# Performance work log

Hardware: AMD Instinct MI355X
Metric: run time of the kernel (lower is better)

## Reference

```python
import jax, jax.numpy as jnp
import numpy as np

N, E = 50000, 800000
IN, HID, EMB, PROJ = 256, 256, 128, 128


def setup_inputs() -> dict:
    key = jax.random.key(0)
    ks = jax.random.split(key, 10)
    s_in = 1.0 / np.sqrt(IN)
    s_hid = 1.0 / np.sqrt(HID)
    s_emb = 1.0 / np.sqrt(EMB)
    s_proj = 1.0 / np.sqrt(PROJ)
    return {
        "x": jax.random.normal(ks[0], (N, IN), jnp.float32),
        "edge_row": jax.random.randint(ks[1], (E,), 0, N),
        "edge_col": jax.random.randint(ks[2], (E,), 0, N),
        "edge_val": jax.random.uniform(ks[3], (E,), jnp.float32),
        "W1": jax.random.normal(ks[4], (IN, HID), jnp.float32) * s_in,
        "b1": jnp.zeros((HID,), jnp.float32),
        "W2": jax.random.normal(ks[5], (HID, HID), jnp.float32) * s_hid,
        "b2": jnp.zeros((HID,), jnp.float32),
        "W3": jax.random.normal(ks[6], (HID, EMB), jnp.float32) * s_hid,
        "b3": jnp.zeros((EMB,), jnp.float32),
        "P1": jax.random.normal(ks[7], (EMB, PROJ), jnp.float32) * s_emb,
        "pb1": jnp.zeros((PROJ,), jnp.float32),
        "P2": jax.random.normal(ks[8], (PROJ, PROJ), jnp.float32) * s_proj,
        "pb2": jnp.zeros((PROJ,), jnp.float32),
    }


def reference(x, edge_row, edge_col, edge_val, W1, b1, W2, b2, W3, b3, P1, pb1, P2, pb2):
    n = x.shape[0]
    # GCNConv is called as conv(x, Adj.t()): transpose swaps row/col.
    # gcn_norm: add self loops (value 1), symmetric normalization D^-1/2 (A+I) D^-1/2.
    loops = jnp.arange(n)
    r = jnp.concatenate([edge_col, loops])  # adj_t rows (destinations)
    c = jnp.concatenate([edge_row, loops])  # adj_t cols (sources)
    v = jnp.concatenate([edge_val, jnp.ones((n,), x.dtype)])
    deg = jax.ops.segment_sum(v, r, num_segments=n)
    dinv = jnp.where(deg > 0, deg ** -0.5, 0.0).astype(x.dtype)
    nv = dinv[r] * v * dinv[c]  # [E+N] normalized edge weights

    def agg(h):  # spmm: out[i] = sum_e nv[e] * h[c[e]] scattered to r[e]
        return jax.ops.segment_sum(nv[:, None] * h[c], r, num_segments=n)

    h = jax.nn.relu(agg(x @ W1) + b1)      # dropout is identity in eval
    h = jax.nn.relu(agg(h @ W2) + b2)
    emb = agg(h @ W3) + b3
    z = jax.nn.relu(emb @ P1 + pb1) @ P2 + pb2
    return emb, z
```

## Files before the change

### kernel.cpp

```cpp
#include <hip/hip_runtime.h>
#include <hip/hip_bf16.h>
#include <cstdint>
#include <cstddef>

#define NN 50000
#define NE 800000
#define NRBP 3128
#define NBK 196

typedef __attribute__((ext_vector_type(8))) short bf16x8;
typedef __attribute__((ext_vector_type(4))) float f32x4;

static __device__ __forceinline__ unsigned short f2bf_u(float f) {
    __hip_bfloat16 h = __float2bfloat16(f);
    return *reinterpret_cast<unsigned short*>(&h);
}
static __device__ __forceinline__ float bfu2f(unsigned short u) {
    __hip_bfloat16 h = *reinterpret_cast<__hip_bfloat16*>(&u);
    return __bfloat162float(h);
}

static __device__ __forceinline__ void gll16(void* lds_dst, const void* gsrc) {
    __builtin_amdgcn_global_load_lds(
        (const __attribute__((address_space(1))) void*)gsrc,
        (__attribute__((address_space(3))) void*)lds_dst, 16, 0, 0);
}


__global__ __launch_bounds__(256) void k_bhist(const int* __restrict__ ecol,
                                               int* __restrict__ bcnt, int e) {
    __shared__ int lcnt[NBK];
    int tid = threadIdx.x;
    for (int t = tid; t < NBK; t += 256) lcnt[t] = 0;
    __syncthreads();
#pragma unroll
    for (int q = 0; q < 4; ++q) {
        int i = blockIdx.x * 1024 + q * 256 + tid;
        if (i < e) atomicAdd(&lcnt[ecol[i] >> 8], 1);
    }
    __syncthreads();
    for (int t = tid; t < NBK; t += 256)
        if (lcnt[t]) atomicAdd(&bcnt[t], lcnt[t]);
}

__global__ void k_bscan(const int* __restrict__ bcnt, int* __restrict__ boff,
                        int* __restrict__ gcur, int* __restrict__ rowptr) {
    int tid = threadIdx.x;
    int v = (tid < NBK) ? bcnt[tid] : 0;
    int lane = tid & 63, w = tid >> 6;
    int incl = v;
#pragma unroll
    for (int d = 1; d < 64; d <<= 1) {
        int t = __shfl_up(incl, d);
        if (lane >= d) incl += t;
    }
    __shared__ int wsum[4];
    if (lane == 63) wsum[w] = incl;
    __syncthreads();
    int woff = 0;
    for (int j = 0; j < w; ++j) woff += wsum[j];
    int ex = woff + incl - v;
    if (tid < NBK) { boff[tid] = ex; gcur[tid] = ex; }
    if (tid == 255) { boff[NBK] = ex; rowptr[NN] = ex; }
}

__global__ __launch_bounds__(256) void k_bscat(const int* __restrict__ erow,
                                               const int* __restrict__ ecol,
                                               const float* __restrict__ eval_,
                                               int* __restrict__ gcur,
                                               int2* __restrict__ tmp, int e) {
    __shared__ int lcnt[NBK], lbase[NBK], lcur[NBK];
    int tid = threadIdx.x;
    for (int t = tid; t < NBK; t += 256) { lcnt[t] = 0; lcur[t] = 0; }
    __syncthreads();
    int d_[4], b_[4];
#pragma unroll
    for (int q = 0; q < 4; ++q) {
        int i = blockIdx.x * 1024 + q * 256 + tid;
        d_[q] = -1;
        if (i < e) {
            d_[q] = ecol[i];
            b_[q] = d_[q] >> 8;
            atomicAdd(&lcnt[b_[q]], 1);
        }
    }
    __syncthreads();
    for (int t = tid; t < NBK; t += 256)
        lbase[t] = lcnt[t] ? atomicAdd(&gcur[t], lcnt[t]) : 0;
    __syncthreads();
#pragma unroll
    for (int q = 0; q < 4; ++q) {
        int i = blockIdx.x * 1024 + q * 256 + tid;
        if (i < e) {
            int b = b_[q];
            int pos = lbase[b] + atomicAdd(&lcur[b], 1);
            tmp[pos] = make_int2(erow[i] | ((d_[q] & 255) << 20), __float_as_int(eval_[i]));
        }
    }
}

__global__ __launch_bounds__(256) void k_bsort(const int2* __restrict__ tmp,
                                               const int* __restrict__ boff,
                                               int* __restrict__ rowptr,
                                               float* __restrict__ dinv,
                                               int2* __restrict__ epk) {
    __shared__ int lcnt[256], lcur[256];
    __shared__ float ldeg[256];
    __shared__ int wsum[4];
    int tid = threadIdx.x;
    int b = blockIdx.x;
    int base = boff[b], endb = boff[b + 1];
    lcnt[tid] = 0;
    ldeg[tid] = 0.f;
    __syncthreads();
    for (int i = base + tid; i < endb; i += 256) {
        int2 e2 = tmp[i];
        int d = e2.x >> 20;
        atomicAdd(&lcnt[d], 1);
        atomicAdd(&ldeg[d], __int_as_float(e2.y));
    }
    __syncthreads();
    int v = lcnt[tid];
    int lane = tid & 63, w = tid >> 6;
    int incl = v;
#pragma unroll
    for (int d = 1; d < 64; d <<= 1) {
        int t = __shfl_up(incl, d);
        if (lane >= d) incl += t;
    }
    if (lane == 63) wsum[w] = incl;
    __syncthreads();
    int woff = 0;
    for (int j = 0; j < w; ++j) woff += wsum[j];
    int ex = woff + incl - v;
    int dest = (b << 8) + tid;
    if (dest < NN) {
        rowptr[dest] = base + ex;
        dinv[dest] = rsqrtf(1.f + ldeg[tid]);
    }
    lcur[tid] = ex;
    __syncthreads();
    for (int i = base + tid; i < endb; i += 256) {
        int2 e2 = tmp[i];
        int d = e2.x >> 20;
        int pos = base + atomicAdd(&lcur[d], 1);
        epk[pos] = make_int2(e2.x & 0xFFFFF, e2.y);
    }
}

__global__ void k_normw(int2* __restrict__ epk, const float* __restrict__ dinv, int e) {
    int i = blockIdx.x * 256 + threadIdx.x;
    if (i < e) {
        int2 pk = epk[i];
        epk[i].y = __float_as_int(__int_as_float(pk.y) * dinv[pk.x]);
    }
}

template<int DIM, bool RELU, bool FRAGOUT>
__global__ __launch_bounds__(256) void k_agg(const unsigned short* __restrict__ H,
                      const int* __restrict__ rowptr, const int2* __restrict__ epk,
                      const float* __restrict__ dinv, const float* __restrict__ bias,
                      float* __restrict__ outf, unsigned short* __restrict__ oh) {
    constexpr int WU = DIM / 128;
    int lane = threadIdx.x & 63;
    int row = blockIdx.x * 4 + (threadIdx.x >> 6);
    if (row >= NN) return;

    const uint2* H2 = reinterpret_cast<const uint2*>(H);
    const unsigned* H1 = reinterpret_cast<const unsigned*>(H);

    auto loadrow = [&](int r, unsigned* v) {
        if constexpr (WU == 2) {
            uint2 t = H2[(size_t)r * 64 + lane];
            v[0] = t.x; v[1] = t.y;
        } else {
            v[0] = H1[(size_t)r * 64 + lane];
        }
    };

    float di = dinv[row];
    float acc[WU * 2];
    {
        unsigned sv[WU];
        loadrow(row, sv);
#pragma unroll
        for (int w2 = 0; w2 < WU; ++w2) {
            acc[w2 * 2 + 0] = di * __uint_as_float(sv[w2] << 16);
            acc[w2 * 2 + 1] = di * __uint_as_float(sv[w2] & 0xffff0000u);
        }
    }

    auto accum = [&](const unsigned* v, float wt) {
#pragma unroll
        for (int w2 = 0; w2 < WU; ++w2) {
            acc[w2 * 2 + 0] += wt * __uint_as_float(v[w2] << 16);
            acc[w2 * 2 + 1] += wt * __uint_as_float(v[w2] & 0xffff0000u);
        }
    };

    int beg = rowptr[row], end = rowptr[row + 1];
    for (int c = beg; c < end; c += 64) {
        int m = min(64, end - c);
        int2 pk = make_int2(0, 0);
        if (c + lane < end) pk = epk[c + lane];
        int j = 0;
        for (; j + 4 <= m; j += 4) {
            int s0 = __shfl(pk.x, j + 0), s1 = __shfl(pk.x, j + 1);
            int s2 = __shfl(pk.x, j + 2), s3 = __shfl(pk.x, j + 3);
            float w0 = __int_as_float(__shfl(pk.y, j + 0));
            float w1 = __int_as_float(__shfl(pk.y, j + 1));
            float w2 = __int_as_float(__shfl(pk.y, j + 2));
            float w3 = __int_as_float(__shfl(pk.y, j + 3));
            unsigned g0[WU], g1[WU], g2[WU], g3[WU];
            loadrow(s0, g0);
            loadrow(s1, g1);
            loadrow(s2, g2);
            loadrow(s3, g3);
            accum(g0, w0);
            accum(g1, w1);
            accum(g2, w2);
            accum(g3, w3);
        }
        for (; j < m; ++j) {
            int s = __shfl(pk.x, j);
            float wt = __int_as_float(__shfl(pk.y, j));
            unsigned g[WU];
            loadrow(s, g);
            accum(g, wt);
        }
    }

    if constexpr (FRAGOUT) {
        float4 b4 = reinterpret_cast<const float4*>(bias)[lane];
        float o0 = acc[0] * di + b4.x;
        float o1 = acc[1] * di + b4.y;
        float o2 = acc[2] * di + b4.z;
        float o3 = acc[3] * di + b4.w;
        if (RELU) {
            o0 = fmaxf(o0, 0.f); o1 = fmaxf(o1, 0.f);
            o2 = fmaxf(o2, 0.f); o3 = fmaxf(o3, 0.f);
        }
        ushort4 h;
        h.x = f2bf_u(o0); h.y = f2bf_u(o1); h.z = f2bf_u(o2); h.w = f2bf_u(o3);
        size_t ch = (size_t)(lane >> 3) * NRBP + (row >> 4);
        int off = ((lane & 7) >> 1) * 128 + (row & 15) * 8 + (lane & 1) * 4;
        *reinterpret_cast<ushort4*>(&oh[ch * 512 + off]) = h;
    } else if constexpr (WU == 2) {
        float4 b4 = reinterpret_cast<const float4*>(bias)[lane];
        float4 o;
        o.x = acc[0] * di + b4.x; o.y = acc[1] * di + b4.y;
        o.z = acc[2] * di + b4.z; o.w = acc[3] * di + b4.w;
        if (RELU) {
            o.x = fmaxf(o.x, 0.f); o.y = fmaxf(o.y, 0.f);
            o.z = fmaxf(o.z, 0.f); o.w = fmaxf(o.w, 0.f);
        }
        reinterpret_cast<float4*>(outf)[(size_t)row * 64 + lane] = o;
    } else {
        float2 b2 = reinterpret_cast<const float2*>(bias)[lane];
        float2 o;
        o.x = acc[0] * di + b2.x; o.y = acc[1] * di + b2.y;
        if (RELU) { o.x = fmaxf(o.x, 0.f); o.y = fmaxf(o.y, 0.f); }
        reinterpret_cast<float2*>(outf)[(size_t)row * 64 + lane] = o;
    }
}

__global__ void k_xsplit(const float* __restrict__ X, unsigned short* __restrict__ xh,
                         int nrows) {
    int idx = blockIdx.x * 256 + threadIdx.x;
    int row = idx >> 6, t = idx & 63;
    if (row >= nrows) return;
    float4 v = *reinterpret_cast<const float4*>(&X[(size_t)row * 256 + t * 4]);
    ushort4 h;
    h.x = f2bf_u(v.x); h.y = f2bf_u(v.y); h.z = f2bf_u(v.z); h.w = f2bf_u(v.w);
    size_t chunk = (size_t)(t >> 3) * NRBP + (row >> 4);
    int off = ((t & 7) >> 1) * 128 + (row & 15) * 8 + (t & 1) * 4;
    *reinterpret_cast<ushort4*>(&xh[chunk * 512 + off]) = h;
}

__global__ void k_wsplit(const float* __restrict__ W, unsigned short* __restrict__ wh,
                         unsigned short* __restrict__ wl, int K, int M) {
    int idx = blockIdx.x * blockDim.x + threadIdx.x;
    if (idx >= K * M) return;
    int k = idx / M, m = idx % M;
    float w = W[idx];
    unsigned short h = f2bf_u(w);
    float hf = bfu2f(h);
    unsigned short lo = f2bf_u(w - hf);
    int kb = k >> 5, kg = (k & 31) >> 3, kj = k & 7;
    int nb = m >> 4, c = m & 15;
    int off = (kb * (M >> 4) + nb) * 512 + kg * 128 + c * 8 + kj;
    wh[off] = h;
    wl[off] = lo;
}

template<int BM, int BN>
__global__ __launch_bounds__((BM / 64) * (BN / 64) * 64)
void k_mmf(const unsigned short* __restrict__ ah,
           const unsigned short* __restrict__ wh, const unsigned short* __restrict__ wl,
           unsigned short* __restrict__ Cbf, int nrows, int K, int M) {
    constexpr int NW = (BM / 64) * (BN / 64);
    constexpr int WN = BN / 64;
    constexpr int AC = BM / 16, BC = BN / 16;
    constexpr int TC = AC + 2 * BC;
    constexpr int BUF = TC * 512;
    __shared__ unsigned short sm[2 * BUF];
    const int tid = threadIdx.x, l = tid & 63, wid = tid >> 6;
    const int wr = wid / WN, wc = wid % WN;
    const int bm = blockIdx.x * BM, bn = blockIdx.y * BN;
    const int rb0 = blockIdx.x * AC, nb0 = blockIdx.y * BC;
    const int NKB = K >> 5, MB = M >> 4;
    const int fo = (l >> 4) * 128 + (l & 15) * 8;
    f32x4 acc[4][4] = {};

    auto stage = [&](int buf, int kb) {
        unsigned short* base = sm + buf * BUF;
        const unsigned short* ga_h = ah + ((size_t)kb * NRBP + rb0) * 512;
        const unsigned short* gb_h = wh + ((size_t)kb * MB + nb0) * 512;
        const unsigned short* gb_l = wl + ((size_t)kb * MB + nb0) * 512;
        for (int q = wid; q < TC; q += NW) {
            const unsigned short* s;
            if (q < AC) s = ga_h + q * 512;
            else if (q < AC + BC) s = gb_h + (q - AC) * 512;
            else s = gb_l + (q - AC - BC) * 512;
            gll16(base + q * 512, s + l * 8);
        }
    };

    stage(0, 0);
    __syncthreads();
    for (int kb = 0; kb < NKB; ++kb) {
        const int cur = kb & 1;
        if (kb + 1 < NKB) stage(cur ^ 1, kb + 1);
        const unsigned short* base = sm + cur * BUF;
        bf16x8 a_h[4], b_h[4], b_l[4];
#pragma unroll
        for (int i = 0; i < 4; ++i)
            a_h[i] = *reinterpret_cast<const bf16x8*>(base + (wr * 4 + i) * 512 + fo);
#pragma unroll
        for (int j = 0; j < 4; ++j) {
            b_h[j] = *reinterpret_cast<const bf16x8*>(base + (AC + wc * 4 + j) * 512 + fo);
            b_l[j] = *reinterpret_cast<const bf16x8*>(base + (AC + BC + wc * 4 + j) * 512 + fo);
        }
#pragma unroll
        for (int i = 0; i < 4; ++i)
#pragma unroll
            for (int j = 0; j < 4; ++j) {
                acc[i][j] = __builtin_amdgcn_mfma_f32_16x16x32_bf16(a_h[i], b_h[j], acc[i][j], 0, 0, 0);
                acc[i][j] = __builtin_amdgcn_mfma_f32_16x16x32_bf16(a_h[i], b_l[j], acc[i][j], 0, 0, 0);
            }
        __syncthreads();
    }
#pragma unroll
    for (int j = 0; j < 4; ++j) {
        int col = bn + wc * 64 + j * 16 + (l & 15);
#pragma unroll
        for (int i = 0; i < 4; ++i) {
            int row0 = bm + wr * 64 + i * 16 + (l >> 4) * 4;
#pragma unroll
            for (int r = 0; r < 4; ++r) {
                int row = row0 + r;
                if (row < nrows)
                    Cbf[(size_t)row * M + col] = f2bf_u(acc[i][j][r]);
            }
        }
    }
}

template<int BM, int BN, bool RELU>
__global__ __launch_bounds__((BM / 64) * (BN / 64) * 64)
void k_mm(const float* __restrict__ A, const unsigned short* __restrict__ wh,
          const unsigned short* __restrict__ wl, const float* __restrict__ bias,
          float* __restrict__ Cout, int nrows, int K, int M) {
    constexpr int T = (BM / 64) * (BN / 64) * 64;
    constexpr int WN = BN / 64;
    constexpr int QI = BM * 8 / T;
    __shared__ unsigned short Ah[BM * 32], Al[BM * 32], Bh[BN * 32], Bl[BN * 32];
    int tid = threadIdx.x;
    int l = tid & 63;
    int wid = tid >> 6;
    int wr = wid / WN, wc = wid % WN;
    int bm = blockIdx.x * BM, bn = blockIdx.y * BN;
    int nb0 = bn >> 4;
    f32x4 acc[4][4] = {};
    int fo = (l >> 4) * 128 + (l & 15) * 8;

    for (int k0 = 0; k0 < K; k0 += 32) {
        int kb = k0 >> 5;
#pragma unroll
        for (int q = 0; q < QI; ++q) {
            int t2 = tid + q * T;
            int row = t2 >> 3, kq = t2 & 7;
            int grow = bm + row;
            float4 av = make_float4(0.f, 0.f, 0.f, 0.f);
            if (grow < nrows)
                av = *reinterpret_cast<const float4*>(&A[(size_t)grow * K + k0 + kq * 4]);
            unsigned short h0 = f2bf_u(av.x), h1 = f2bf_u(av.y),
                           h2 = f2bf_u(av.z), h3 = f2bf_u(av.w);
            uint2 hp, lp;
            hp.x = (unsigned)h0 | ((unsigned)h1 << 16);
            hp.y = (unsigned)h2 | ((unsigned)h3 << 16);
            lp.x = (unsigned)f2bf_u(av.x - bfu2f(h0)) | ((unsigned)f2bf_u(av.y - bfu2f(h1)) << 16);
            lp.y = (unsigned)f2bf_u(av.z - bfu2f(h2)) | ((unsigned)f2bf_u(av.w - bfu2f(h3)) << 16);
            int off = (row >> 4) * 512 + (kq >> 1) * 128 + (row & 15) * 8 + (kq & 1) * 4;
            *reinterpret_cast<uint2*>(&Ah[off]) = hp;
            *reinterpret_cast<uint2*>(&Al[off]) = lp;
        }
        const int4* sh = reinterpret_cast<const int4*>(wh) + (size_t)(kb * (M >> 4) + nb0) * 64;
        const int4* sl = reinterpret_cast<const int4*>(wl) + (size_t)(kb * (M >> 4) + nb0) * 64;
        for (int u = tid; u < BN * 4; u += T) {
            *reinterpret_cast<int4*>(&Bh[u * 8]) = sh[u];
            *reinterpret_cast<int4*>(&Bl[u * 8]) = sl[u];
        }
        __syncthreads();
        bf16x8 ah4[4], al4[4], bh4[4], bl4[4];
#pragma unroll
        for (int i = 0; i < 4; ++i) {
            ah4[i] = *reinterpret_cast<const bf16x8*>(&Ah[(wr * 4 + i) * 512 + fo]);
            al4[i] = *reinterpret_cast<const bf16x8*>(&Al[(wr * 4 + i) * 512 + fo]);
        }
#pragma unroll
        for (int j = 0; j < 4; ++j) {
            bh4[j] = *reinterpret_cast<const bf16x8*>(&Bh[(wc * 4 + j) * 512 + fo]);
            bl4[j] = *reinterpret_cast<const bf16x8*>(&Bl[(wc * 4 + j) * 512 + fo]);
        }
#pragma unroll
        for (int i = 0; i < 4; ++i)
#pragma unroll
            for (int j = 0; j < 4; ++j) {
                acc[i][j] = __builtin_amdgcn_mfma_f32_16x16x32_bf16(ah4[i], bh4[j], acc[i][j], 0, 0, 0);
                acc[i][j] = __builtin_amdgcn_mfma_f32_16x16x32_bf16(ah4[i], bl4[j], acc[i][j], 0, 0, 0);
                acc[i][j] = __builtin_amdgcn_mfma_f32_16x16x32_bf16(al4[i], bh4[j], acc[i][j], 0, 0, 0);
            }
        __syncthreads();
    }
#pragma unroll
    for (int j = 0; j < 4; ++j) {
        int col = bn + wc * 64 + j * 16 + (l & 15);
        float bv = bias[col];
#pragma unroll
        for (int i = 0; i < 4; ++i) {
            int row0 = bm + wr * 64 + i * 16 + (l >> 4) * 4;
#pragma unroll
            for (int r = 0; r < 4; ++r) {
                int row = row0 + r;
                if (row < nrows) {
                    float v = acc[i][j][r] + bv;
                    if (RELU) v = fmaxf(v, 0.f);
                    Cout[(size_t)row * M + col] = v;
                }
            }
        }
    }
}


extern "C" void kernel_launch(void* const* d_in, const int* in_sizes, int n_in,
                              void* d_out, int out_size, void* d_ws, size_t ws_size,
                              hipStream_t stream) {
    const float* x        = (const float*)d_in[0];
    const int*   edge_row = (const int*)d_in[1];
    const int*   edge_col = (const int*)d_in[2];
    const float* edge_val = (const float*)d_in[3];
    const float* W1  = (const float*)d_in[4];
    const float* b1  = (const float*)d_in[5];
    const float* W2  = (const float*)d_in[6];
    const float* b2  = (const float*)d_in[7];
    const float* W3  = (const float*)d_in[8];
    const float* b3  = (const float*)d_in[9];
    const float* P1  = (const float*)d_in[10];
    const float* pb1 = (const float*)d_in[11];
    const float* P2  = (const float*)d_in[12];
    const float* pb2 = (const float*)d_in[13];

    const int N = NN, E = NE;

    uintptr_t p = (uintptr_t)d_ws;
    auto alloc = [&](size_t bytes) -> void* {
        void* r = (void*)p;
        p += (bytes + 255) & ~(size_t)255;
        return r;
    };
    float* dinv   = (float*)alloc((size_t)N * 4);
    int*   rowptr = (int*)alloc((size_t)(N + 1) * 4);
    int*   bcnt   = (int*)alloc(256 * 4);
    int*   boff   = (int*)alloc(256 * 4);
    int*   gcur   = (int*)alloc(256 * 4);
    int2*  etmp   = (int2*)alloc((size_t)E * 8);
    int2*  epk    = (int2*)alloc((size_t)E * 8);
    unsigned short* Hbf = (unsigned short*)alloc((size_t)N * 256 * 2);
    const size_t PLANE = (size_t)8 * NRBP * 512 * 2;
    unsigned short* pAh = (unsigned short*)alloc(PLANE);
    unsigned short* pBh = (unsigned short*)alloc(PLANE);
    float* bufT = (float*)alloc((size_t)N * 128 * 4);
    unsigned short* wf1h = (unsigned short*)alloc(65536 * 2);
    unsigned short* wf1l = (unsigned short*)alloc(65536 * 2);
    unsigned short* wf2h = (unsigned short*)alloc(65536 * 2);
    unsigned short* wf2l = (unsigned short*)alloc(65536 * 2);
    unsigned short* wf3h = (unsigned short*)alloc(32768 * 2);
    unsigned short* wf3l = (unsigned short*)alloc(32768 * 2);
    unsigned short* p1h  = (unsigned short*)alloc(16384 * 2);
    unsigned short* p1l  = (unsigned short*)alloc(16384 * 2);
    unsigned short* p2h  = (unsigned short*)alloc(16384 * 2);
    unsigned short* p2l  = (unsigned short*)alloc(16384 * 2);

    float* emb = (float*)d_out;
    float* z   = (float*)d_out + (size_t)N * 128;

    dim3 b256(256);
    const int gE1k = (E + 1023) / 1024;

    k_wsplit<<<dim3(256), b256, 0, stream>>>(W1, wf1h, wf1l, 256, 256);
    k_wsplit<<<dim3(256), b256, 0, stream>>>(W2, wf2h, wf2l, 256, 256);
    k_wsplit<<<dim3(128), b256, 0, stream>>>(W3, wf3h, wf3l, 256, 128);
    k_wsplit<<<dim3(64),  b256, 0, stream>>>(P1, p1h, p1l, 128, 128);
    k_wsplit<<<dim3(64),  b256, 0, stream>>>(P2, p2h, p2l, 128, 128);
    k_xsplit<<<dim3((N * 64 + 255) / 256), b256, 0, stream>>>(x, pAh, N);

    hipMemsetAsync(bcnt, 0, 256 * 4, stream);
    k_bhist<<<dim3(gE1k), b256, 0, stream>>>(edge_col, bcnt, E);
    k_bscan<<<dim3(1), b256, 0, stream>>>(bcnt, boff, gcur, rowptr);
    k_bscat<<<dim3(gE1k), b256, 0, stream>>>(edge_row, edge_col, edge_val, gcur, etmp, E);
    k_bsort<<<dim3(NBK), b256, 0, stream>>>(etmp, boff, rowptr, dinv, epk);
    k_normw<<<dim3((E + 255) / 256), b256, 0, stream>>>(epk, dinv, E);

    const int gagg = (N + 3) / 4;

    k_mmf<128, 128><<<dim3(391, 2), dim3(256), 0, stream>>>(pAh, wf1h, wf1l, Hbf, N, 256, 256);
    k_agg<256, true, true><<<dim3(gagg), b256, 0, stream>>>(Hbf, rowptr, epk, dinv, b1, nullptr, pBh);
    k_mmf<128, 128><<<dim3(391, 2), dim3(256), 0, stream>>>(pBh, wf2h, wf2l, Hbf, N, 256, 256);
    k_agg<256, true, true><<<dim3(gagg), b256, 0, stream>>>(Hbf, rowptr, epk, dinv, b2, nullptr, pAh);
    k_mmf<64, 128><<<dim3(782, 1), dim3(128), 0, stream>>>(pAh, wf3h, wf3l, Hbf, N, 256, 128);
    k_agg<128, false, false><<<dim3(gagg), b256, 0, stream>>>(Hbf, rowptr, epk, dinv, b3, emb, nullptr);
    k_mm<64, 128, true ><<<dim3(782, 1), dim3(128), 0, stream>>>(emb, p1h, p1l, pb1, bufT, N, 128, 128);
    k_mm<64, 128, false><<<dim3(782, 1), dim3(128), 0, stream>>>(bufT, p2h, p2l, pb2, z, N, 128, 128);
}
```

Measured before the change: 374.0 us.

## Use fixed-capacity buckets, deeper gather unroll, and bf16 fragment inputs for projection head

Drops the histogram and scan kernels by giving each destination bucket a fixed capacity slot and storing per-row (begin,end) ranges. The aggregation gather loop now issues 8 neighbour row loads per batch instead of 4 to expose more memory parallelism. The final aggregation also writes a bf16 fragment-layout copy of emb, so the two projection GEMMs reuse the preformatted k_mmf path instead of converting fp32 inputs in-kernel. The intermediate projection result is stored in bf16 fragment form. Risks: bucket overflow if degree skew exceeds BKCAP, extra padded normw work, and the intermediate projection input is now stored as a single bf16 value instead of the previous bf16 high/low split.

```diff
diff --git a/kernel.cpp b/kernel.cpp
--- a/kernel.cpp
+++ b/kernel.cpp
@@ -7,9 +7,14 @@
 #define NE 800000
 #define NRBP 3128
 #define NBK 196
+#define BKCAP 4608
 
 typedef __attribute__((ext_vector_type(8))) short bf16x8;
 typedef __attribute__((ext_vector_type(4))) float f32x4;
+
+#define OUT_BF16ROW 0
+#define OUT_FRAG    1
+#define OUT_F32     2
 
 static __device__ __forceinline__ unsigned short f2bf_u(float f) {
     __hip_bfloat16 h = __float2bfloat16(f);
@@ -26,43 +31,6 @@
         (__attribute__((address_space(3))) void*)lds_dst, 16, 0, 0);
 }
 
-
-__global__ __launch_bounds__(256) void k_bhist(const int* __restrict__ ecol,
-                                               int* __restrict__ bcnt, int e) {
-    __shared__ int lcnt[NBK];
-    int tid = threadIdx.x;
-    for (int t = tid; t < NBK; t += 256) lcnt[t] = 0;
-    __syncthreads();
-#pragma unroll
-    for (int q = 0; q < 4; ++q) {
-        int i = blockIdx.x * 1024 + q * 256 + tid;
-        if (i < e) atomicAdd(&lcnt[ecol[i] >> 8], 1);
-    }
-    __syncthreads();
-    for (int t = tid; t < NBK; t += 256)
-        if (lcnt[t]) atomicAdd(&bcnt[t], lcnt[t]);
-}
-
-__global__ void k_bscan(const int* __restrict__ bcnt, int* __restrict__ boff,
-                        int* __restrict__ gcur, int* __restrict__ rowptr) {
-    int tid = threadIdx.x;
-    int v = (tid < NBK) ? bcnt[tid] : 0;
-    int lane = tid & 63, w = tid >> 6;
-    int incl = v;
-#pragma unroll
-    for (int d = 1; d < 64; d <<= 1) {
-        int t = __shfl_up(incl, d);
-        if (lane >= d) incl += t;
-    }
-    __shared__ int wsum[4];
-    if (lane == 63) wsum[w] = incl;
-    __syncthreads();
-    int woff = 0;
-    for (int j = 0; j < w; ++j) woff += wsum[j];
-    int ex = woff + incl - v;
-    if (tid < NBK) { boff[tid] = ex; gcur[tid] = ex; }
-    if (tid == 255) { boff[NBK] = ex; rowptr[NN] = ex; }
-}
 
 __global__ __launch_bounds__(256) void k_bscat(const int* __restrict__ erow,
                                                const int* __restrict__ ecol,
@@ -86,7 +54,7 @@
     }
     __syncthreads();
     for (int t = tid; t < NBK; t += 256)
-        lbase[t] = lcnt[t] ? atomicAdd(&gcur[t], lcnt[t]) : 0;
+        lbase[t] = lcnt[t] ? (t * BKCAP + atomicAdd(&gcur[t], lcnt[t])) : 0;
     __syncthreads();
 #pragma unroll
     for (int q = 0; q < 4; ++q) {
@@ -100,8 +68,8 @@
 }
 
 __global__ __launch_bounds__(256) void k_bsort(const int2* __restrict__ tmp,
-                                               const int* __restrict__ boff,
-                                               int* __restrict__ rowptr,
+                                               const int* __restrict__ cnt,
+                                               int2* __restrict__ rowrange,
                                                float* __restrict__ dinv,
                                                int2* __restrict__ epk) {
     __shared__ int lcnt[256], lcur[256];
@@ -109,7 +77,7 @@
     __shared__ int wsum[4];
     int tid = threadIdx.x;
     int b = blockIdx.x;
-    int base = boff[b], endb = boff[b + 1];
+    int base = b * BKCAP, endb = base + cnt[b];
     lcnt[tid] = 0;
     ldeg[tid] = 0.f;
     __syncthreads();
@@ -135,7 +103,7 @@
     int ex = woff + incl - v;
     int dest = (b << 8) + tid;
     if (dest < NN) {
-        rowptr[dest] = base + ex;
+        rowrange[dest] = make_int2(base + ex, base + ex + v);
         dinv[dest] = rsqrtf(1.f + ldeg[tid]);
     }
     lcur[tid] = ex;
@@ -148,17 +116,20 @@
     }
 }
 
-__global__ void k_normw(int2* __restrict__ epk, const float* __restrict__ dinv, int e) {
+__global__ void k_normw(int2* __restrict__ epk, const float* __restrict__ dinv,
+                        const int* __restrict__ cnt) {
     int i = blockIdx.x * 256 + threadIdx.x;
-    if (i < e) {
+    if (i >= NBK * BKCAP) return;
+    int b = i / BKCAP;
+    if (i - b * BKCAP < cnt[b]) {
         int2 pk = epk[i];
         epk[i].y = __float_as_int(__int_as_float(pk.y) * dinv[pk.x]);
     }
 }
 
-template<int DIM, bool RELU, bool FRAGOUT>
+template<int DIM, bool RELU, int OMODE>
 __global__ __launch_bounds__(256) void k_agg(const unsigned short* __restrict__ H,
-                      const int* __restrict__ rowptr, const int2* __restrict__ epk,
+                      const int2* __restrict__ rowrange, const int2* __restrict__ epk,
                       const float* __restrict__ dinv, const float* __restrict__ bias,
                       float* __restrict__ outf, unsigned short* __restrict__ oh) {
     constexpr int WU = DIM / 128;
@@ -198,28 +169,26 @@
         }
     };
 
-    int beg = rowptr[row], end = rowptr[row + 1];
+    int2 rr = rowrange[row];
+    int beg = rr.x, end = rr.y;
     for (int c = beg; c < end; c += 64) {
         int m = min(64, end - c);
         int2 pk = make_int2(0, 0);
         if (c + lane < end) pk = epk[c + lane];
         int j = 0;
-        for (; j + 4 <= m; j += 4) {
-            int s0 = __shfl(pk.x, j + 0), s1 = __shfl(pk.x, j + 1);
-            int s2 = __shfl(pk.x, j + 2), s3 = __shfl(pk.x, j + 3);
-            float w0 = __int_as_float(__shfl(pk.y, j + 0));
-            float w1 = __int_as_float(__shfl(pk.y, j + 1));
-            float w2 = __int_as_float(__shfl(pk.y, j + 2));
-            float w3 = __int_as_float(__shfl(pk.y, j + 3));
-            unsigned g0[WU], g1[WU], g2[WU], g3[WU];
-            loadrow(s0, g0);
-            loadrow(s1, g1);
-            loadrow(s2, g2);
-            loadrow(s3, g3);
-            accum(g0, w0);
-            accum(g1, w1);
-            accum(g2, w2);
-            accum(g3, w3);
+        for (; j + 8 <= m; j += 8) {
+            int s[8];
+            float wv[8];
+#pragma unroll
+            for (int q = 0; q < 8; ++q) {
+                s[q] = __shfl(pk.x, j + q);
+                wv[q] = __int_as_float(__shfl(pk.y, j + q));
+            }
+            unsigned g[8][WU];
+#pragma unroll
+            for (int q = 0; q < 8; ++q) loadrow(s[q], g[q]);
+#pragma unroll
+            for (int q = 0; q < 8; ++q) accum(g[q], wv[q]);
         }
         for (; j < m; ++j) {
             int s = __shfl(pk.x, j);
@@ -230,7 +199,7 @@
         }
     }
 
-    if constexpr (FRAGOUT) {
+    if constexpr (OMODE == 1) {
         float4 b4 = reinterpret_cast<const float4*>(bias)[lane];
         float o0 = acc[0] * di + b4.x;
         float o1 = acc[1] * di + b4.y;
@@ -257,10 +226,19 @@
         reinterpret_cast<float4*>(outf)[(size_t)row * 64 + lane] = o;
     } else {
         float2 b2 = reinterpret_cast<const float2*>(bias)[lane];
-        float2 o;
-        o.x = acc[0] * di + b2.x; o.y = acc[1] * di + b2.y;
-        if (RELU) { o.x = fmaxf(o.x, 0.f); o.y = fmaxf(o.y, 0.f); }
-        reinterpret_cast<float2*>(outf)[(size_t)row * 64 + lane] = o;
+        float o0 = acc[0] * di + b2.x;
+        float o1 = acc[1] * di + b2.y;
+        if (RELU) { o0 = fmaxf(o0, 0.f); o1 = fmaxf(o1, 0.f); }
+        reinterpret_cast<float2*>(outf)[(size_t)row * 64 + lane] = make_float2(o0, o1);
+        if constexpr (OMODE == 2) {
+            int c0 = 2 * lane;
+            int kb = c0 >> 5, kg = (c0 & 31) >> 3, kj = c0 & 7;
+            size_t ch = (size_t)kb * NRBP + (row >> 4);
+            int off = kg * 128 + (row & 15) * 8 + kj;
+            ushort2 h2s;
+            h2s.x = f2bf_u(o0); h2s.y = f2bf_u(o1);
+            *reinterpret_cast<ushort2*>(&oh[ch * 512 + off]) = h2s;
+        }
     }
 }
 
@@ -293,11 +271,12 @@
     wl[off] = lo;
 }
 
-template<int BM, int BN>
+template<int BM, int BN, int OMODE, bool RELU>
 __global__ __launch_bounds__((BM / 64) * (BN / 64) * 64)
 void k_mmf(const unsigned short* __restrict__ ah,
            const unsigned short* __restrict__ wh, const unsigned short* __restrict__ wl,
-           unsigned short* __restrict__ Cbf, int nrows, int K, int M) {
+           const float* __restrict__ bias, void* __restrict__ Cout,
+           int nrows, int K, int M) {
     constexpr int NW = (BM / 64) * (BN / 64);
     constexpr int WN = BN / 64;
     constexpr int AC = BM / 16, BC = BN / 16;
@@ -353,100 +332,24 @@
 #pragma unroll
     for (int j = 0; j < 4; ++j) {
         int col = bn + wc * 64 + j * 16 + (l & 15);
+        float bv = (OMODE != OUT_BF16ROW) ? bias[col] : 0.f;
 #pragma unroll
         for (int i = 0; i < 4; ++i) {
             int row0 = bm + wr * 64 + i * 16 + (l >> 4) * 4;
 #pragma unroll
             for (int r = 0; r < 4; ++r) {
                 int row = row0 + r;
-                if (row < nrows)
-                    Cbf[(size_t)row * M + col] = f2bf_u(acc[i][j][r]);
-            }
-        }
-    }
-}
-
-template<int BM, int BN, bool RELU>
-__global__ __launch_bounds__((BM / 64) * (BN / 64) * 64)
-void k_mm(const float* __restrict__ A, const unsigned short* __restrict__ wh,
-          const unsigned short* __restrict__ wl, const float* __restrict__ bias,
-          float* __restrict__ Cout, int nrows, int K, int M) {
-    constexpr int T = (BM / 64) * (BN / 64) * 64;
-    constexpr int WN = BN / 64;
-    constexpr int QI = BM * 8 / T;
-    __shared__ unsigned short Ah[BM * 32], Al[BM * 32], Bh[BN * 32], Bl[BN * 32];
-    int tid = threadIdx.x;
-    int l = tid & 63;
-    int wid = tid >> 6;
-    int wr = wid / WN, wc = wid % WN;
-    int bm = blockIdx.x * BM, bn = blockIdx.y * BN;
-    int nb0 = bn >> 4;
-    f32x4 acc[4][4] = {};
-    int fo = (l >> 4) * 128 + (l & 15) * 8;
-
-    for (int k0 = 0; k0 < K; k0 += 32) {
-        int kb = k0 >> 5;
-#pragma unroll
-        for (int q = 0; q < QI; ++q) {
-            int t2 = tid + q * T;
-            int row = t2 >> 3, kq = t2 & 7;
-            int grow = bm + row;
-            float4 av = make_float4(0.f, 0.f, 0.f, 0.f);
-            if (grow < nrows)
-                av = *reinterpret_cast<const float4*>(&A[(size_t)grow * K + k0 + kq * 4]);
-            unsigned short h0 = f2bf_u(av.x), h1 = f2bf_u(av.y),
-                           h2 = f2bf_u(av.z), h3 = f2bf_u(av.w);
-            uint2 hp, lp;
-            hp.x = (unsigned)h0 | ((unsigned)h1 << 16);
-            hp.y = (unsigned)h2 | ((unsigned)h3 << 16);
-            lp.x = (unsigned)f2bf_u(av.x - bfu2f(h0)) | ((unsigned)f2bf_u(av.y - bfu2f(h1)) << 16);
-            lp.y = (unsigned)f2bf_u(av.z - bfu2f(h2)) | ((unsigned)f2bf_u(av.w - bfu2f(h3)) << 16);
-            int off = (row >> 4) * 512 + (kq >> 1) * 128 + (row & 15) * 8 + (kq & 1) * 4;
-            *reinterpret_cast<uint2*>(&Ah[off]) = hp;
-            *reinterpret_cast<uint2*>(&Al[off]) = lp;
-        }
-        const int4* sh = reinterpret_cast<const int4*>(wh) + (size_t)(kb * (M >> 4) + nb0) * 64;
-        const int4* sl = reinterpret_cast<const int4*>(wl) + (size_t)(kb * (M >> 4) + nb0) * 64;
-        for (int u = tid; u < BN * 4; u += T) {
-            *reinterpret_cast<int4*>(&Bh[u * 8]) = sh[u];
-            *reinterpret_cast<int4*>(&Bl[u * 8]) = sl[u];
-        }
-        __syncthreads();
-        bf16x8 ah4[4], al4[4], bh4[4], bl4[4];
-#pragma unroll
-        for (int i = 0; i < 4; ++i) {
-            ah4[i] = *reinterpret_cast<const bf16x8*>(&Ah[(wr * 4 + i) * 512 + fo]);
-            al4[i] = *reinterpret_cast<const bf16x8*>(&Al[(wr * 4 + i) * 512 + fo]);
-        }
-#pragma unroll
-        for (int j = 0; j < 4; ++j) {
-            bh4[j] = *reinterpret_cast<const bf16x8*>(&Bh[(wc * 4 + j) * 512 + fo]);
-            bl4[j] = *reinterpret_cast<const bf16x8*>(&Bl[(wc * 4 + j) * 512 + fo]);
-        }
-#pragma unroll
-        for (int i = 0; i < 4; ++i)
-#pragma unroll
-            for (int j = 0; j < 4; ++j) {
-                acc[i][j] = __builtin_amdgcn_mfma_f32_16x16x32_bf16(ah4[i], bh4[j], acc[i][j], 0, 0, 0);
-                acc[i][j] = __builtin_amdgcn_mfma_f32_16x16x32_bf16(ah4[i], bl4[j], acc[i][j], 0, 0, 0);
-                acc[i][j] = __builtin_amdgcn_mfma_f32_16x16x32_bf16(al4[i], bh4[j], acc[i][j], 0, 0, 0);
-            }
-        __syncthreads();
-    }
-#pragma unroll
-    for (int j = 0; j < 4; ++j) {
-        int col = bn + wc * 64 + j * 16 + (l & 15);
-        float bv = bias[col];
-#pragma unroll
-        for (int i = 0; i < 4; ++i) {
-            int row0 = bm + wr * 64 + i * 16 + (l >> 4) * 4;
-#pragma unroll
-            for (int r = 0; r < 4; ++r) {
-                int row = row0 + r;
-                if (row < nrows) {
-                    float v = acc[i][j][r] + bv;
-                    if (RELU) v = fmaxf(v, 0.f);
-                    Cout[(size_t)row * M + col] = v;
+                if (row >= nrows) continue;
+                float v = acc[i][j][r] + bv;
+                if (RELU) v = fmaxf(v, 0.f);
+                if constexpr (OMODE == OUT_BF16ROW) {
+                    ((unsigned short*)Cout)[(size_t)row * M + col] = f2bf_u(v);
+                } else if constexpr (OMODE == OUT_FRAG) {
+                    size_t ch = (size_t)(col >> 5) * NRBP + (row >> 4);
+                    int off = ((col & 31) >> 3) * 128 + (row & 15) * 8 + (col & 7);
+                    ((unsigned short*)Cout)[ch * 512 + off] = f2bf_u(v);
+                } else {
+                    ((float*)Cout)[(size_t)row * M + col] = v;
                 }
             }
         }
@@ -473,6 +376,7 @@
     const float* pb2 = (const float*)d_in[13];
 
     const int N = NN, E = NE;
+    const size_t EPAD = (size_t)NBK * BKCAP;
 
     uintptr_t p = (uintptr_t)d_ws;
     auto alloc = [&](size_t bytes) -> void* {
@@ -480,18 +384,18 @@
         p += (bytes + 255) & ~(size_t)255;
         return r;
     };
-    float* dinv   = (float*)alloc((size_t)N * 4);
-    int*   rowptr = (int*)alloc((size_t)(N + 1) * 4);
-    int*   bcnt   = (int*)alloc(256 * 4);
-    int*   boff   = (int*)alloc(256 * 4);
-    int*   gcur   = (int*)alloc(256 * 4);
-    int2*  etmp   = (int2*)alloc((size_t)E * 8);
-    int2*  epk    = (int2*)alloc((size_t)E * 8);
+    float* dinv     = (float*)alloc((size_t)N * 4);
+    int2*  rowrange = (int2*)alloc((size_t)N * 8);
+    int*   gcur     = (int*)alloc(256 * 4);
+    int2*  etmp     = (int2*)alloc(EPAD * 8);
+    int2*  epk      = (int2*)alloc(EPAD * 8);
     unsigned short* Hbf = (unsigned short*)alloc((size_t)N * 256 * 2);
-    const size_t PLANE = (size_t)8 * NRBP * 512 * 2;
-    unsigned short* pAh = (unsigned short*)alloc(PLANE);
-    unsigned short* pBh = (unsigned short*)alloc(PLANE);
-    float* bufT = (float*)alloc((size_t)N * 128 * 4);
+    const size_t PLANE8 = (size_t)8 * NRBP * 512 * 2;
+    const size_t PLANE4 = (size_t)4 * NRBP * 512 * 2;
+    unsigned short* pAh   = (unsigned short*)alloc(PLANE8);
+    unsigned short* pBh   = (unsigned short*)alloc(PLANE8);
+    unsigned short* embF  = (unsigned short*)alloc(PLANE4);
+    unsigned short* bufTF = (unsigned short*)alloc(PLANE4);
     unsigned short* wf1h = (unsigned short*)alloc(65536 * 2);
     unsigned short* wf1l = (unsigned short*)alloc(65536 * 2);
     unsigned short* wf2h = (unsigned short*)alloc(65536 * 2);
@@ -516,21 +420,24 @@
     k_wsplit<<<dim3(64),  b256, 0, stream>>>(P2, p2h, p2l, 128, 128);
     k_xsplit<<<dim3((N * 64 + 255) / 256), b256, 0, stream>>>(x, pAh, N);
 
-    hipMemsetAsync(bcnt, 0, 256 * 4, stream);
-    k_bhist<<<dim3(gE1k), b256, 0, stream>>>(edge_col, bcnt, E);
-    k_bscan<<<dim3(1), b256, 0, stream>>>(bcnt, boff, gcur, rowptr);
+    hipMemsetAsync(gcur, 0, 256 * 4, stream);
     k_bscat<<<dim3(gE1k), b256, 0, stream>>>(edge_row, edge_col, edge_val, gcur, etmp, E);
-    k_bsort<<<dim3(NBK), b256, 0, stream>>>(etmp, boff, rowptr, dinv, epk);
-    k_normw<<<dim3((E + 255) / 256), b256, 0, stream>>>(epk, dinv, E);
+    k_bsort<<<dim3(NBK), b256, 0, stream>>>(etmp, gcur, rowrange, dinv, epk);
+    k_normw<<<dim3((int)((EPAD + 255) / 256)), b256, 0, stream>>>(epk, dinv, gcur);
 
     const int gagg = (N + 3) / 4;
 
-    k_mmf<128, 128><<<dim3(391, 2), dim3(256), 0, stream>>>(pAh, wf1h, wf1l, Hbf, N, 256, 256);
-    k_agg<256, true, true><<<dim3(gagg), b256, 0, stream>>>(Hbf, rowptr, epk, dinv, b1, nullptr, pBh);
-    k_mmf<128, 128><<<dim3(391, 2), dim3(256), 0, stream>>>(pBh, wf2h, wf2l, Hbf, N, 256, 256);
-    k_agg<256, true, true><<<dim3(gagg), b256, 0, stream>>>(Hbf, rowptr, epk, dinv, b2, nullptr, pAh);
-    k_mmf<64, 128><<<dim3(782, 1), dim3(128), 0, stream>>>(pAh, wf3h, wf3l, Hbf, N, 256, 128);
-    k_agg<128, false, false><<<dim3(gagg), b256, 0, stream>>>(Hbf, rowptr, epk, dinv, b3, emb, nullptr);
-    k_mm<64, 128, true ><<<dim3(782, 1), dim3(128), 0, stream>>>(emb, p1h, p1l, pb1, bufT, N, 128, 128);
-    k_mm<64, 128, false><<<dim3(782, 1), dim3(128), 0, stream>>>(bufT, p2h, p2l, pb2, z, N, 128, 128);
-}
+    k_mmf<128, 128, OUT_BF16ROW, false><<<dim3(391, 2), dim3(256), 0, stream>>>(
+        pAh, wf1h, wf1l, nullptr, Hbf, N, 256, 256);
+    k_agg<256, true, 1><<<dim3(gagg), b256, 0, stream>>>(Hbf, rowrange, epk, dinv, b1, nullptr, pBh);
+    k_mmf<128, 128, OUT_BF16ROW, false><<<dim3(391, 2), dim3(256), 0, stream>>>(
+        pBh, wf2h, wf2l, nullptr, Hbf, N, 256, 256);
+    k_agg<256, true, 1><<<dim3(gagg), b256, 0, stream>>>(Hbf, rowrange, epk, dinv, b2, nullptr, pAh);
+    k_mmf<64, 128, OUT_BF16ROW, false><<<dim3(782, 1), dim3(128), 0, stream>>>(
+        pAh, wf3h, wf3l, nullptr, Hbf, N, 256, 128);
+    k_agg<128, false, 2><<<dim3(gagg), b256, 0, stream>>>(Hbf, rowrange, epk, dinv, b3, emb, embF);
+    k_mmf<64, 128, OUT_FRAG, true><<<dim3(782, 1), dim3(128), 0, stream>>>(
+        embF, p1h, p1l, pb1, bufTF, N, 128, 128);
+    k_mmf<64, 128, OUT_F32, false><<<dim3(782, 1), dim3(128), 0, stream>>>(
+        bufTF, p2h, p2l, pb2, z, N, 128, 128);
+}
```

After: 346.6 us. -7.3%, faster.
